# Optimization experiments

Measured on AMD Instinct MI355X. Metric: run time of the kernel, lower is better.

Reference implementation:

```python
import jax, jax.numpy as jnp
import numpy as np

DEPTH = 3
DIM = 64
N_NODES = 4096
BATCH = 4


def setup_inputs() -> dict:
    key = jax.random.key(0)
    k1, k2, k3, k4 = jax.random.split(key, 4)
    x = jax.random.normal(k1, (BATCH, N_NODES, DIM), dtype=jnp.float32)
    graph = jax.random.uniform(k2, (BATCH, N_NODES, N_NODES), dtype=jnp.float32)
    # Linear((depth+1)*dim, dim): PyTorch default init U(-1/sqrt(fan_in), 1/sqrt(fan_in))
    fan_in = (DEPTH + 1) * DIM
    bound = 1.0 / np.sqrt(fan_in)
    W = jax.random.uniform(k3, (DIM, fan_in), minval=-bound, maxval=bound, dtype=jnp.float32)
    b = jax.random.uniform(k4, (DIM,), minval=-bound, maxval=bound, dtype=jnp.float32)
    return {"x": x, "graph": graph, "W": W, "b": b}


def reference(x, graph, W, b):
    # GCN branch of LocalGNN.forward (dropout p=0 -> identity).
    n = graph.shape[-1]
    g = graph + jnp.eye(n, dtype=graph.dtype)          # add self loops
    d = 1.0 / (jnp.sqrt(g.sum(axis=-1)) + 1e-7)        # [b, n]
    # D @ g @ D with D = diag(d):  g_ij * d_i * d_j
    g = g * d[..., :, None] * d[..., None, :]
    outs = [x]
    h = x
    for _ in range(DEPTH):
        h = jnp.einsum('bij,bjd->bid', g, h)           # dense propagation
        outs.append(h)
    cat = jnp.concatenate(outs, axis=-1)               # [b, n, (depth+1)*dim]
    return cat @ W.T + b
```

## Files before the change

kernel.cpp:

```cpp
#include <hip/hip_runtime.h>
#include <hip/hip_bf16.h>


typedef __attribute__((ext_vector_type(4))) float  floatx4;
typedef __attribute__((ext_vector_type(8))) short  short8;

#define NB 4
#define NN 4096
#define ND 64
#define KSPLIT 4
#define HSZ ((size_t)NB * NN * ND)

__device__ __forceinline__ unsigned short f2bf_bits(float v) {
    __hip_bfloat16 b = __float2bfloat16(v);
    return *reinterpret_cast<unsigned short*>(&b);
}

__device__ __forceinline__ short8 pack8(floatx4 a, floatx4 b) {
    short8 r;
    r[0] = (short)f2bf_bits(a[0]); r[1] = (short)f2bf_bits(a[1]);
    r[2] = (short)f2bf_bits(a[2]); r[3] = (short)f2bf_bits(a[3]);
    r[4] = (short)f2bf_bits(b[0]); r[5] = (short)f2bf_bits(b[1]);
    r[6] = (short)f2bf_bits(b[2]); r[7] = (short)f2bf_bits(b[3]);
    return r;
}

__global__ void rowsum_kernel(const float* __restrict__ graph, float* __restrict__ dinv) {
    int row = blockIdx.x;
    const float* g = graph + (size_t)row * NN;
    int t = threadIdx.x;
    float s = 0.f;
#pragma unroll
    for (int q = 0; q < 4; ++q) {
        floatx4 v = *reinterpret_cast<const floatx4*>(g + q * 1024 + t * 4);
        s += v[0] + v[1] + v[2] + v[3];
    }
#pragma unroll
    for (int off = 32; off > 0; off >>= 1) s += __shfl_down(s, off);
    __shared__ float wsum[4];
    if ((t & 63) == 0) wsum[t >> 6] = s;
    __syncthreads();
    if (t == 0) {
        float tot = wsum[0] + wsum[1] + wsum[2] + wsum[3] + 1.0f;
        dinv[row] = 1.0f / (sqrtf(tot) + 1e-7f);
    }
}

__global__ void make_ghat(const float* __restrict__ g, const float* __restrict__ dinv,
                          unsigned short* __restrict__ ghat) {
    size_t e = ((size_t)blockIdx.x * 256 + threadIdx.x) * 16;
    int ig = (int)(e >> 12);
    int b  = ig >> 12;
    int i  = ig & 4095;
    int j0 = (int)(e & 4095);
    float di = dinv[ig];
    const float* dj = dinv + (size_t)b * NN + j0;
    const float* gp = g + e;
    floatx4 v[4], d[4];
#pragma unroll
    for (int q = 0; q < 4; ++q) {
        v[q] = *reinterpret_cast<const floatx4*>(gp + q * 4);
        d[q] = *reinterpret_cast<const floatx4*>(dj + q * 4);
    }
    if (i >= j0 && i < j0 + 16) {
        float* vf = (float*)v;
        vf[i - j0] += 1.0f;
    }
#pragma unroll
    for (int q = 0; q < 4; ++q) v[q] = v[q] * d[q] * di;
    short8 o0 = pack8(v[0], v[1]);
    short8 o1 = pack8(v[2], v[3]);
    *reinterpret_cast<short8*>(ghat + e)     = o0;
    *reinterpret_cast<short8*>(ghat + e + 8) = o1;
}

__global__ void castT_kernel(const float* __restrict__ src, unsigned short* __restrict__ hT) {
    __shared__ float tile[64][65];
    int b = blockIdx.y, row0 = blockIdx.x * 64;
    size_t base = ((size_t)b * NN + row0) * ND;
#pragma unroll
    for (int qi = 0; qi < 16; ++qi) {
        int idx = qi * 256 + threadIdx.x;
        tile[idx >> 6][idx & 63] = src[base + idx];
    }
    __syncthreads();
#pragma unroll
    for (int qi = 0; qi < 16; ++qi) {
        int idx = qi * 256 + threadIdx.x;
        int n = idx >> 6, r = idx & 63;
        hT[((size_t)b * ND + n) * NN + row0 + r] = f2bf_bits(tile[r][n]);
    }
}

__global__ __launch_bounds__(256) void prop_gemm(const unsigned short* __restrict__ ghat,
                                                 const unsigned short* __restrict__ hT,
                                                 float* __restrict__ P) {
    __shared__ __align__(16) unsigned short Bs[64][72];
    int bid  = blockIdx.x;
    int b    = bid & 3;
    int ks   = (bid >> 2) & 3;
    int mblk = bid >> 4;
    int w    = threadIdx.x >> 6;
    int lane = threadIdx.x & 63;
    int m = lane & 15, q = lane >> 4;
    int row0 = mblk * 128 + w * 32;
    int k0 = ks * 1024;

    const unsigned short* A0 = ghat + (size_t)b * NN * NN + (size_t)(row0 + m) * NN + k0 + q * 8;
    const unsigned short* A1 = A0 + (size_t)16 * NN;

    int t = threadIdx.x;
    int sn = t >> 2, sk = (t & 3) * 16;
    const unsigned short* src = hT + (size_t)b * ND * NN + (size_t)sn * NN + k0 + sk;

    floatx4 acc[2][4];
#pragma unroll
    for (int mt = 0; mt < 2; ++mt)
#pragma unroll
        for (int c = 0; c < 4; ++c) acc[mt][c] = (floatx4){0.f, 0.f, 0.f, 0.f};

    short8 v0 = *reinterpret_cast<const short8*>(src);
    short8 v1 = *reinterpret_cast<const short8*>(src + 8);

    for (int kk = 0; kk < 1024; kk += 64) {
        __syncthreads();
        *reinterpret_cast<short8*>(&Bs[sn][sk])     = v0;
        *reinterpret_cast<short8*>(&Bs[sn][sk + 8]) = v1;
        __syncthreads();
        if (kk + 64 < 1024) {
            src += 64;
            v0 = *reinterpret_cast<const short8*>(src);
            v1 = *reinterpret_cast<const short8*>(src + 8);
        }
#pragma unroll
        for (int ki = 0; ki < 2; ++ki) {
            short8 a0 = *reinterpret_cast<const short8*>(A0 + kk + ki * 32);
            short8 a1 = *reinterpret_cast<const short8*>(A1 + kk + ki * 32);
#pragma unroll
            for (int c = 0; c < 4; ++c) {
                short8 bf = *reinterpret_cast<const short8*>(&Bs[c * 16 + m][ki * 32 + q * 8]);
                acc[0][c] = __builtin_amdgcn_mfma_f32_16x16x32_bf16(a0, bf, acc[0][c], 0, 0, 0);
                acc[1][c] = __builtin_amdgcn_mfma_f32_16x16x32_bf16(a1, bf, acc[1][c], 0, 0, 0);
            }
        }
    }

    float* pout = P + ((size_t)ks * NB + b) * ((size_t)NN * ND);
#pragma unroll
    for (int mt = 0; mt < 2; ++mt)
#pragma unroll
        for (int c = 0; c < 4; ++c)
#pragma unroll
            for (int r = 0; r < 4; ++r) {
                int row = row0 + mt * 16 + q * 4 + r;
                pout[(size_t)row * ND + c * 16 + m] = acc[mt][c][r];
            }
}

__global__ void prep_kernel(const float* __restrict__ P,
                            unsigned short* __restrict__ hrow,
                            unsigned short* __restrict__ hT) {
    __shared__ float tile[64][65];
    int b = blockIdx.y, row0 = blockIdx.x * 64;
    size_t base = ((size_t)b * NN + row0) * ND;
    const size_t SZ = HSZ;
#pragma unroll
    for (int qi = 0; qi < 16; ++qi) {
        int idx = qi * 256 + threadIdx.x;
        int r = idx >> 6, n = idx & 63;
        size_t off = base + idx;
        float s = P[off] + P[SZ + off] + P[2 * SZ + off] + P[3 * SZ + off];
        hrow[off] = f2bf_bits(s);
        tile[r][n] = s;
    }
    __syncthreads();
#pragma unroll
    for (int qi = 0; qi < 16; ++qi) {
        int idx = qi * 256 + threadIdx.x;
        int n = idx >> 6, r = idx & 63;
        hT[((size_t)b * ND + n) * NN + row0 + r] = f2bf_bits(tile[r][n]);
    }
}

__global__ __launch_bounds__(256) void final_linear(const float* __restrict__ x,
                                                    const unsigned short* __restrict__ h1,
                                                    const unsigned short* __restrict__ h2,
                                                    const unsigned short* __restrict__ h3,
                                                    const float* __restrict__ W,
                                                    const float* __restrict__ bias,
                                                    float* __restrict__ out) {
    int wid  = blockIdx.x * 4 + (threadIdx.x >> 6);
    int lane = threadIdx.x & 63;
    int b = wid >> 8;
    int row0 = (wid & 255) * 16;
    int m = lane & 15, q = lane >> 4;

    floatx4 acc[4];
#pragma unroll
    for (int c = 0; c < 4; ++c) acc[c] = (floatx4){0.f, 0.f, 0.f, 0.f};

    {
        const float* A = x + ((size_t)b * NN + row0 + m) * ND;
#pragma unroll
        for (int ki = 0; ki < 2; ++ki) {
            floatx4 a0 = *reinterpret_cast<const floatx4*>(A + ki * 32 + q * 8);
            floatx4 a1 = *reinterpret_cast<const floatx4*>(A + ki * 32 + q * 8 + 4);
            short8 af = pack8(a0, a1);
#pragma unroll
            for (int c = 0; c < 4; ++c) {
                const float* Wr = W + (size_t)(c * 16 + m) * 256 + ki * 32 + q * 8;
                short8 bf = pack8(*reinterpret_cast<const floatx4*>(Wr),
                                  *reinterpret_cast<const floatx4*>(Wr + 4));
                acc[c] = __builtin_amdgcn_mfma_f32_16x16x32_bf16(af, bf, acc[c], 0, 0, 0);
            }
        }
    }
    const unsigned short* hs[3] = {h1, h2, h3};
#pragma unroll
    for (int p = 1; p < 4; ++p) {
        const unsigned short* A = hs[p - 1] + ((size_t)b * NN + row0 + m) * ND;
#pragma unroll
        for (int ki = 0; ki < 2; ++ki) {
            short8 af = *reinterpret_cast<const short8*>(A + ki * 32 + q * 8);
#pragma unroll
            for (int c = 0; c < 4; ++c) {
                const float* Wr = W + (size_t)(c * 16 + m) * 256 + p * 64 + ki * 32 + q * 8;
                short8 bf = pack8(*reinterpret_cast<const floatx4*>(Wr),
                                  *reinterpret_cast<const floatx4*>(Wr + 4));
                acc[c] = __builtin_amdgcn_mfma_f32_16x16x32_bf16(af, bf, acc[c], 0, 0, 0);
            }
        }
    }
#pragma unroll
    for (int c = 0; c < 4; ++c) {
        float bb = bias[c * 16 + m];
#pragma unroll
        for (int r = 0; r < 4; ++r) {
            int row = row0 + q * 4 + r;
            out[((size_t)b * NN + row) * ND + c * 16 + m] = acc[c][r] + bb;
        }
    }
}

extern "C" void kernel_launch(void* const* d_in, const int* in_sizes, int n_in,
                              void* d_out, int out_size, void* d_ws, size_t ws_size,
                              hipStream_t stream) {
    const float* x     = (const float*)d_in[0];
    const float* graph = (const float*)d_in[1];
    const float* W     = (const float*)d_in[2];
    const float* bias  = (const float*)d_in[3];
    float* out = (float*)d_out;

    char* w = (char*)d_ws;
    float*          dinv = (float*)w;
    unsigned short* hT   = (unsigned short*)(w + (1 << 16));
    unsigned short* ghat = (unsigned short*)(w + (1 << 16) + (1 << 21));
    char* w2 = w + (1 << 16) + (1 << 21) + ((size_t)NB * NN * NN * 2);
    float*          P    = (float*)w2;
    unsigned short* h1   = (unsigned short*)(w2 + KSPLIT * HSZ * 4);
    unsigned short* h2   = h1 + HSZ;
    unsigned short* h3   = h2 + HSZ;

    rowsum_kernel<<<NB * NN, 256, 0, stream>>>(graph, dinv);
    make_ghat<<<(NB * NN * NN) / (256 * 16), 256, 0, stream>>>(graph, dinv, ghat);
    castT_kernel<<<dim3(NN / 64, NB), 256, 0, stream>>>(x, hT);

    unsigned short* houts[3] = {h1, h2, h3};
    for (int s = 0; s < 3; ++s) {
        prop_gemm<<<512, 256, 0, stream>>>(ghat, hT, P);
        prep_kernel<<<dim3(NN / 64, NB), 256, 0, stream>>>(P, houts[s], hT);
    }
    final_linear<<<256, 256, 0, stream>>>(x, h1, h2, h3, W, bias, out);
}
```

Baseline: 560.8 us.

## Pre-swizzle ghat and h into MFMA fragment order, drop LDS staging in prop_gemm

The normalized graph is written in a fragment-swizzled layout, so each wave in prop_gemm loads its MFMA A operand with one contiguous 16-byte-per-lane load. The feature matrix is likewise stored in B-fragment order by castF/prep, which removes the LDS staging and __syncthreads from the propagation GEMM. Each wave now owns a 16-row tile with a 4-way K split, giving 1024 blocks in place of 512. In exchange, make_ghat gains an LDS tile and a strided write pattern, and each wave gets less reuse per A load than the previous 32-row tile.

```diff
diff --git a/kernel.cpp b/kernel.cpp
--- a/kernel.cpp
+++ b/kernel.cpp
@@ -8,20 +8,18 @@
 #define NB 4
 #define NN 4096
 #define ND 64
-#define KSPLIT 4
 #define HSZ ((size_t)NB * NN * ND)
+#define HF_B 262144
 
 __device__ __forceinline__ unsigned short f2bf_bits(float v) {
     __hip_bfloat16 b = __float2bfloat16(v);
     return *reinterpret_cast<unsigned short*>(&b);
 }
 
-__device__ __forceinline__ short8 pack8(floatx4 a, floatx4 b) {
+__device__ __forceinline__ short8 pack8p(const float* v) {
     short8 r;
-    r[0] = (short)f2bf_bits(a[0]); r[1] = (short)f2bf_bits(a[1]);
-    r[2] = (short)f2bf_bits(a[2]); r[3] = (short)f2bf_bits(a[3]);
-    r[4] = (short)f2bf_bits(b[0]); r[5] = (short)f2bf_bits(b[1]);
-    r[6] = (short)f2bf_bits(b[2]); r[7] = (short)f2bf_bits(b[3]);
+#pragma unroll
+    for (int j = 0; j < 8; ++j) r[j] = (short)f2bf_bits(v[j]);
     return r;
 }
 
@@ -46,127 +44,133 @@
     }
 }
 
-__global__ void make_ghat(const float* __restrict__ g, const float* __restrict__ dinv,
-                          unsigned short* __restrict__ ghat) {
-    size_t e = ((size_t)blockIdx.x * 256 + threadIdx.x) * 16;
-    int ig = (int)(e >> 12);
-    int b  = ig >> 12;
-    int i  = ig & 4095;
-    int j0 = (int)(e & 4095);
-    float di = dinv[ig];
-    const float* dj = dinv + (size_t)b * NN + j0;
-    const float* gp = g + e;
-    floatx4 v[4], d[4];
-#pragma unroll
-    for (int q = 0; q < 4; ++q) {
-        v[q] = *reinterpret_cast<const floatx4*>(gp + q * 4);
-        d[q] = *reinterpret_cast<const floatx4*>(dj + q * 4);
-    }
-    if (i >= j0 && i < j0 + 16) {
-        float* vf = (float*)v;
-        vf[i - j0] += 1.0f;
-    }
-#pragma unroll
-    for (int q = 0; q < 4; ++q) v[q] = v[q] * d[q] * di;
-    short8 o0 = pack8(v[0], v[1]);
-    short8 o1 = pack8(v[2], v[3]);
-    *reinterpret_cast<short8*>(ghat + e)     = o0;
-    *reinterpret_cast<short8*>(ghat + e + 8) = o1;
-}
-
-__global__ void castT_kernel(const float* __restrict__ src, unsigned short* __restrict__ hT) {
+__global__ __launch_bounds__(256) void make_ghat_sw(const float* __restrict__ g,
+                                                    const float* __restrict__ dinv,
+                                                    unsigned short* __restrict__ gsw) {
+    __shared__ float tile[16][524];
+    int bid = blockIdx.x;
+    int b = bid >> 8, mt = bid & 255;
+    int t = threadIdx.x;
+    const float* grow  = g + ((size_t)b * NN + mt * 16) * NN;
+    const float* dinvb = dinv + (size_t)b * NN;
+    size_t outbase = (((size_t)(b * 256 + mt)) * 128) * 512;
+
+    for (int s0 = 0; s0 < NN; s0 += 512) {
+        __syncthreads();
+#pragma unroll
+        for (int li = 0; li < 8; ++li) {
+            int flat = li * 1024 + t * 4;
+            int r = flat >> 9, cidx = flat & 511;
+            floatx4 v = *reinterpret_cast<const floatx4*>(grow + (size_t)r * NN + s0 + cidx);
+            *reinterpret_cast<floatx4*>(&tile[r][cidx]) = v;
+        }
+        __syncthreads();
+#pragma unroll
+        for (int gg = 0; gg < 4; ++gg) {
+            int gi = gg * 256 + t;
+            int kcl = gi >> 6;
+            int ln  = gi & 63;
+            int m = ln & 15, q = ln >> 4;
+            int i_row = mt * 16 + m;
+            float di = dinvb[i_row];
+            int kbase = s0 + kcl * 32 + q * 8;
+            floatx4 dj0 = *reinterpret_cast<const floatx4*>(dinvb + kbase);
+            floatx4 dj1 = *reinterpret_cast<const floatx4*>(dinvb + kbase + 4);
+            float v[8];
+#pragma unroll
+            for (int j = 0; j < 8; ++j) {
+                float xv = tile[m][kcl * 32 + q * 8 + j];
+                if (kbase + j == i_row) xv += 1.0f;
+                float dj = (j < 4) ? dj0[j] : dj1[j - 4];
+                v[j] = xv * di * dj;
+            }
+            short8 o = pack8p(v);
+            size_t kc = (size_t)(s0 >> 5) + kcl;
+            *reinterpret_cast<short8*>(gsw + outbase + kc * 512 + ln * 8) = o;
+        }
+    }
+}
+
+__global__ void castF_kernel(const float* __restrict__ x, unsigned short* __restrict__ hF) {
     __shared__ float tile[64][65];
     int b = blockIdx.y, row0 = blockIdx.x * 64;
     size_t base = ((size_t)b * NN + row0) * ND;
+    int t = threadIdx.x;
 #pragma unroll
     for (int qi = 0; qi < 16; ++qi) {
-        int idx = qi * 256 + threadIdx.x;
-        tile[idx >> 6][idx & 63] = src[base + idx];
+        int idx = qi * 256 + t;
+        tile[idx >> 6][idx & 63] = x[base + idx];
     }
     __syncthreads();
 #pragma unroll
-    for (int qi = 0; qi < 16; ++qi) {
-        int idx = qi * 256 + threadIdx.x;
-        int n = idx >> 6, r = idx & 63;
-        hT[((size_t)b * ND + n) * NN + row0 + r] = f2bf_bits(tile[r][n]);
-    }
-}
-
-__global__ __launch_bounds__(256) void prop_gemm(const unsigned short* __restrict__ ghat,
-                                                 const unsigned short* __restrict__ hT,
-                                                 float* __restrict__ P) {
-    __shared__ __align__(16) unsigned short Bs[64][72];
-    int bid  = blockIdx.x;
-    int b    = bid & 3;
-    int ks   = (bid >> 2) & 3;
-    int mblk = bid >> 4;
-    int w    = threadIdx.x >> 6;
+    for (int gg = 0; gg < 2; ++gg) {
+        int gi = gg * 256 + t;
+        int kcl = gi >> 8;
+        int c   = (gi >> 6) & 3;
+        int ln  = gi & 63;
+        int m = ln & 15, q = ln >> 4;
+        float v[8];
+#pragma unroll
+        for (int j = 0; j < 8; ++j) v[j] = tile[kcl * 32 + q * 8 + j][c * 16 + m];
+        short8 o = pack8p(v);
+        size_t kc = (size_t)blockIdx.x * 2 + kcl;
+        *reinterpret_cast<short8*>(hF + (size_t)b * HF_B + ((kc * 4 + c) * 64 + ln) * 8) = o;
+    }
+}
+
+__global__ __launch_bounds__(256, 4) void prop_gemm(const unsigned short* __restrict__ gsw,
+                                                    const unsigned short* __restrict__ hF,
+                                                    float* __restrict__ P) {
+    int wid  = blockIdx.x * 4 + (threadIdx.x >> 6);
     int lane = threadIdx.x & 63;
+    int b  = wid >> 10;
+    int ks = (wid >> 8) & 3;
+    int mt = wid & 255;
     int m = lane & 15, q = lane >> 4;
-    int row0 = mblk * 128 + w * 32;
-    int k0 = ks * 1024;
-
-    const unsigned short* A0 = ghat + (size_t)b * NN * NN + (size_t)(row0 + m) * NN + k0 + q * 8;
-    const unsigned short* A1 = A0 + (size_t)16 * NN;
-
-    int t = threadIdx.x;
-    int sn = t >> 2, sk = (t & 3) * 16;
-    const unsigned short* src = hT + (size_t)b * ND * NN + (size_t)sn * NN + k0 + sk;
-
-    floatx4 acc[2][4];
-#pragma unroll
-    for (int mt = 0; mt < 2; ++mt)
-#pragma unroll
-        for (int c = 0; c < 4; ++c) acc[mt][c] = (floatx4){0.f, 0.f, 0.f, 0.f};
-
-    short8 v0 = *reinterpret_cast<const short8*>(src);
-    short8 v1 = *reinterpret_cast<const short8*>(src + 8);
-
-    for (int kk = 0; kk < 1024; kk += 64) {
-        __syncthreads();
-        *reinterpret_cast<short8*>(&Bs[sn][sk])     = v0;
-        *reinterpret_cast<short8*>(&Bs[sn][sk + 8]) = v1;
-        __syncthreads();
-        if (kk + 64 < 1024) {
-            src += 64;
-            v0 = *reinterpret_cast<const short8*>(src);
-            v1 = *reinterpret_cast<const short8*>(src + 8);
-        }
-#pragma unroll
-        for (int ki = 0; ki < 2; ++ki) {
-            short8 a0 = *reinterpret_cast<const short8*>(A0 + kk + ki * 32);
-            short8 a1 = *reinterpret_cast<const short8*>(A1 + kk + ki * 32);
-#pragma unroll
-            for (int c = 0; c < 4; ++c) {
-                short8 bf = *reinterpret_cast<const short8*>(&Bs[c * 16 + m][ki * 32 + q * 8]);
-                acc[0][c] = __builtin_amdgcn_mfma_f32_16x16x32_bf16(a0, bf, acc[0][c], 0, 0, 0);
-                acc[1][c] = __builtin_amdgcn_mfma_f32_16x16x32_bf16(a1, bf, acc[1][c], 0, 0, 0);
-            }
-        }
+
+    const unsigned short* Ap = gsw + (((size_t)(b * 256 + mt)) * 128 + ks * 32) * 512 + lane * 8;
+    const unsigned short* Bp = hF + (size_t)b * HF_B + (size_t)(ks * 32) * 2048 + lane * 8;
+
+    floatx4 acc0 = {0.f,0.f,0.f,0.f}, acc1 = acc0, acc2 = acc0, acc3 = acc0;
+
+#pragma unroll 2
+    for (int kc = 0; kc < 32; ++kc) {
+        short8 a  = *reinterpret_cast<const short8*>(Ap);
+        short8 b0 = *reinterpret_cast<const short8*>(Bp);
+        short8 b1 = *reinterpret_cast<const short8*>(Bp + 512);
+        short8 b2 = *reinterpret_cast<const short8*>(Bp + 1024);
+        short8 b3 = *reinterpret_cast<const short8*>(Bp + 1536);
+        Ap += 512;
+        Bp += 2048;
+        acc0 = __builtin_amdgcn_mfma_f32_16x16x32_bf16(a, b0, acc0, 0, 0, 0);
+        acc1 = __builtin_amdgcn_mfma_f32_16x16x32_bf16(a, b1, acc1, 0, 0, 0);
+        acc2 = __builtin_amdgcn_mfma_f32_16x16x32_bf16(a, b2, acc2, 0, 0, 0);
+        acc3 = __builtin_amdgcn_mfma_f32_16x16x32_bf16(a, b3, acc3, 0, 0, 0);
     }
 
     float* pout = P + ((size_t)ks * NB + b) * ((size_t)NN * ND);
-#pragma unroll
-    for (int mt = 0; mt < 2; ++mt)
-#pragma unroll
-        for (int c = 0; c < 4; ++c)
-#pragma unroll
-            for (int r = 0; r < 4; ++r) {
-                int row = row0 + mt * 16 + q * 4 + r;
-                pout[(size_t)row * ND + c * 16 + m] = acc[mt][c][r];
-            }
+    int row0 = mt * 16;
+    floatx4* accs[4] = {&acc0, &acc1, &acc2, &acc3};
+#pragma unroll
+    for (int c = 0; c < 4; ++c)
+#pragma unroll
+        for (int r = 0; r < 4; ++r) {
+            int row = row0 + q * 4 + r;
+            pout[(size_t)row * ND + c * 16 + m] = (*accs[c])[r];
+        }
 }
 
 __global__ void prep_kernel(const float* __restrict__ P,
                             unsigned short* __restrict__ hrow,
-                            unsigned short* __restrict__ hT) {
+                            unsigned short* __restrict__ hF) {
     __shared__ float tile[64][65];
     int b = blockIdx.y, row0 = blockIdx.x * 64;
     size_t base = ((size_t)b * NN + row0) * ND;
     const size_t SZ = HSZ;
+    int t = threadIdx.x;
 #pragma unroll
     for (int qi = 0; qi < 16; ++qi) {
-        int idx = qi * 256 + threadIdx.x;
+        int idx = qi * 256 + t;
         int r = idx >> 6, n = idx & 63;
         size_t off = base + idx;
         float s = P[off] + P[SZ + off] + P[2 * SZ + off] + P[3 * SZ + off];
@@ -175,10 +179,18 @@
     }
     __syncthreads();
 #pragma unroll
-    for (int qi = 0; qi < 16; ++qi) {
-        int idx = qi * 256 + threadIdx.x;
-        int n = idx >> 6, r = idx & 63;
-        hT[((size_t)b * ND + n) * NN + row0 + r] = f2bf_bits(tile[r][n]);
+    for (int gg = 0; gg < 2; ++gg) {
+        int gi = gg * 256 + t;
+        int kcl = gi >> 8;
+        int c   = (gi >> 6) & 3;
+        int ln  = gi & 63;
+        int m = ln & 15, q = ln >> 4;
+        float v[8];
+#pragma unroll
+        for (int j = 0; j < 8; ++j) v[j] = tile[kcl * 32 + q * 8 + j][c * 16 + m];
+        short8 o = pack8p(v);
+        size_t kc = (size_t)blockIdx.x * 2 + kcl;
+        *reinterpret_cast<short8*>(hF + (size_t)b * HF_B + ((kc * 4 + c) * 64 + ln) * 8) = o;
     }
 }
 
@@ -203,14 +215,17 @@
         const float* A = x + ((size_t)b * NN + row0 + m) * ND;
 #pragma unroll
         for (int ki = 0; ki < 2; ++ki) {
-            floatx4 a0 = *reinterpret_cast<const floatx4*>(A + ki * 32 + q * 8);
-            floatx4 a1 = *reinterpret_cast<const floatx4*>(A + ki * 32 + q * 8 + 4);
-            short8 af = pack8(a0, a1);
+            float av[8];
+#pragma unroll
+            for (int j = 0; j < 8; ++j) av[j] = A[ki * 32 + q * 8 + j];
+            short8 af = pack8p(av);
 #pragma unroll
             for (int c = 0; c < 4; ++c) {
                 const float* Wr = W + (size_t)(c * 16 + m) * 256 + ki * 32 + q * 8;
-                short8 bf = pack8(*reinterpret_cast<const floatx4*>(Wr),
-                                  *reinterpret_cast<const floatx4*>(Wr + 4));
+                float wv[8];
+#pragma unroll
+                for (int j = 0; j < 8; ++j) wv[j] = Wr[j];
+                short8 bf = pack8p(wv);
                 acc[c] = __builtin_amdgcn_mfma_f32_16x16x32_bf16(af, bf, acc[c], 0, 0, 0);
             }
         }
@@ -225,8 +240,10 @@
 #pragma unroll
             for (int c = 0; c < 4; ++c) {
                 const float* Wr = W + (size_t)(c * 16 + m) * 256 + p * 64 + ki * 32 + q * 8;
-                short8 bf = pack8(*reinterpret_cast<const floatx4*>(Wr),
-                                  *reinterpret_cast<const floatx4*>(Wr + 4));
+                float wv[8];
+#pragma unroll
+                for (int j = 0; j < 8; ++j) wv[j] = Wr[j];
+                short8 bf = pack8p(wv);
                 acc[c] = __builtin_amdgcn_mfma_f32_16x16x32_bf16(af, bf, acc[c], 0, 0, 0);
             }
         }
@@ -253,22 +270,22 @@
 
     char* w = (char*)d_ws;
     float*          dinv = (float*)w;
-    unsigned short* hT   = (unsigned short*)(w + (1 << 16));
-    unsigned short* ghat = (unsigned short*)(w + (1 << 16) + (1 << 21));
+    unsigned short* hF   = (unsigned short*)(w + (1 << 16));
+    unsigned short* gsw  = (unsigned short*)(w + (1 << 16) + (1 << 21));
     char* w2 = w + (1 << 16) + (1 << 21) + ((size_t)NB * NN * NN * 2);
     float*          P    = (float*)w2;
-    unsigned short* h1   = (unsigned short*)(w2 + KSPLIT * HSZ * 4);
+    unsigned short* h1   = (unsigned short*)(w2 + 4 * HSZ * 4);
     unsigned short* h2   = h1 + HSZ;
     unsigned short* h3   = h2 + HSZ;
 
     rowsum_kernel<<<NB * NN, 256, 0, stream>>>(graph, dinv);
-    make_ghat<<<(NB * NN * NN) / (256 * 16), 256, 0, stream>>>(graph, dinv, ghat);
-    castT_kernel<<<dim3(NN / 64, NB), 256, 0, stream>>>(x, hT);
+    make_ghat_sw<<<NB * 256, 256, 0, stream>>>(graph, dinv, gsw);
+    castF_kernel<<<dim3(NN / 64, NB), 256, 0, stream>>>(x, hF);
 
     unsigned short* houts[3] = {h1, h2, h3};
     for (int s = 0; s < 3; ++s) {
-        prop_gemm<<<512, 256, 0, stream>>>(ghat, hT, P);
-        prep_kernel<<<dim3(NN / 64, NB), 256, 0, stream>>>(P, houts[s], hT);
+        prop_gemm<<<1024, 256, 0, stream>>>(gsw, hF, P);
+        prep_kernel<<<dim3(NN / 64, NB), 256, 0, stream>>>(P, houts[s], hF);
     }
     final_linear<<<256, 256, 0, stream>>>(x, h1, h2, h3, W, bias, out);
 }
```

Result: slower. 591.4 us (+5.5%).
